# Optimization experiments

Measured on AMD Instinct MI355X. Metric: run time of the kernel, lower is better.

The kernel has to match this reference:

```python
import jax, jax.numpy as jnp
import numpy as np

R, B, N, H = 10, 8, 8192, 8          # ROIs, patients, nodes/ROI-graph, inner hidden
K = N // 2                            # TopKPooling ratio=0.5 -> ceil(0.5*N)
EPAIR = 65536                         # undirected edge pairs per patient graph
E = 2 * B * EPAIR                     # directed edges per ROI (both directions, all patients)
FIN = 4
HEADS, OH = 4, 16
SUPER_DIM = 2 * H + 3                 # (inner_layers+1)*hidden + 3 centroid coords = 19
EPS = 1e-5


def setup_inputs() -> dict:
    key = jax.random.key(0)
    ks = jax.random.split(key, 24)
    roi_x = jax.random.normal(ks[0], (R, B * N, FIN), jnp.float32)
    # within-graph undirected random edges, offset per patient
    u = jax.random.randint(ks[1], (R, B, EPAIR), 0, N)
    v = jax.random.randint(ks[2], (R, B, EPAIR), 0, N)
    off = (jnp.arange(B) * N)[None, :, None]
    src = jnp.concatenate([u + off, v + off], axis=-1).reshape(R, -1)
    dst = jnp.concatenate([v + off, u + off], axis=-1).reshape(R, -1)
    roi_edge_index = jnp.stack([src, dst], axis=1).astype(jnp.int32)  # [R, 2, E]
    centroids = jax.random.uniform(ks[3], (R, B, 3), jnp.float32) + 0.1  # nonzero -> all ROIs kept
    g = lambda k, s: jax.random.normal(k, s, jnp.float32) * 0.1
    return {
        'roi_x': roi_x,
        'roi_edge_index': roi_edge_index,
        'centroids': centroids,
        'gcn_w': g(ks[4], (R, FIN, H)),
        'gcn_b': g(ks[5], (R, H)),
        'ln_w': jnp.ones((R, H), jnp.float32),
        'ln_b': jnp.zeros((R, H), jnp.float32),
        'topk_w': g(ks[6], (R, H)),
        'gat1_w': g(ks[7], (SUPER_DIM, HEADS * OH)),
        'att_src1': g(ks[8], (HEADS, OH)),
        'att_dst1': g(ks[9], (HEADS, OH)),
        'gat1_b': g(ks[10], (HEADS * OH,)),
        'ln_o1_w': jnp.ones((HEADS * OH,), jnp.float32),
        'ln_o1_b': jnp.zeros((HEADS * OH,), jnp.float32),
        'gat2_w': g(ks[11], (HEADS * OH, OH)),
        'att_src2': g(ks[12], (1, OH)),
        'att_dst2': g(ks[13], (1, OH)),
        'gat2_b': g(ks[14], (OH,)),
        'ln_o2_w': jnp.ones((OH,), jnp.float32),
        'ln_o2_b': jnp.zeros((OH,), jnp.float32),
        'lin_w': g(ks[15], (OH, 2)),
        'lin_b': g(ks[16], (2,)),
    }


def _inner_roi(x, edges, cen, Wg, bg, wln, bln, wtk):
    """GCNConv(4,H)+ReLU -> graph-mode LayerNorm -> TopKPooling -> mean pools. x: [B*N, 4]."""
    src, dst = edges[0], edges[1]
    h = x @ Wg                                                     # [BN, H]
    # GCN symmetric norm with self loops: deg = in-degree + 1
    deg = jax.ops.segment_sum(jnp.ones((E,), x.dtype), dst, num_segments=B * N) + 1.0
    dis = deg ** -0.5
    norm = dis[src] * dis[dst]
    agg = jax.ops.segment_sum(h[src] * norm[:, None], dst, num_segments=B * N)
    h = jax.nn.relu(agg + h / deg[:, None] + bg)
    # PyG LayerNorm (mode='graph'): normalize over all nodes & channels per patient graph
    hb = h.reshape(B, N, H)
    mu = hb.mean(axis=(1, 2), keepdims=True)
    var = ((hb - mu) ** 2).mean(axis=(1, 2), keepdims=True)
    hn = (hb - mu) / jnp.sqrt(var + EPS) * wln + bln               # [B, N, H]
    res = hn.mean(axis=1)                                          # residual global_mean_pool [B, H]
    # TopKPooling: score = tanh(x.w/||w||); keep top K per graph; scale kept nodes by score
    s = jnp.tanh(jnp.einsum('bnh,h->bn', hn, wtk) / jnp.linalg.norm(wtk))
    vals, idx = jax.lax.top_k(s, K)                                # [B, K]
    sel = jnp.take_along_axis(hn, idx[:, :, None], axis=1) * vals[:, :, None]
    fv = sel.mean(axis=1)                                          # global_mean_pool after pooling
    return jnp.concatenate([res, fv, cen], axis=1)                 # [B, 19]


def _gat(x, src, dst, W, a_s, a_d, b, heads, oc):
    """PyG GATConv (self loops already included in src/dst)."""
    n = x.shape[0]
    h = (x @ W).reshape(n, heads, oc)
    es = (h * a_s).sum(-1)                                         # [n, heads]
    ed = (h * a_d).sum(-1)
    e = jax.nn.leaky_relu(es[src] + ed[dst], 0.2)                  # [E, heads]
    m = jax.ops.segment_max(e, dst, num_segments=n)
    ex = jnp.exp(e - m[dst])
    den = jax.ops.segment_sum(ex, dst, num_segments=n)
    alpha = ex / den[dst]
    out = jax.ops.segment_sum(h[src] * alpha[:, :, None], dst, num_segments=n)
    return out.reshape(n, heads * oc) + b


def _graph_ln(x, w, b):
    xb = x.reshape(B, R, -1)
    mu = xb.mean(axis=(1, 2), keepdims=True)
    var = ((xb - mu) ** 2).mean(axis=(1, 2), keepdims=True)
    return ((xb - mu) / jnp.sqrt(var + EPS) * w + b).reshape(B * R, -1)


def reference(roi_x, roi_edge_index, centroids, gcn_w, gcn_b, ln_w, ln_b, topk_w,
              gat1_w, att_src1, att_dst1, gat1_b, ln_o1_w, ln_o1_b,
              gat2_w, att_src2, att_dst2, gat2_b, ln_o2_w, ln_o2_b, lin_w, lin_b):
    feats = jax.vmap(_inner_roi)(roi_x, roi_edge_index, centroids,
                                 gcn_w, gcn_b, ln_w, ln_b, topk_w)   # [R, B, 19]
    super_x = feats.transpose(1, 0, 2).reshape(B * R, SUPER_DIM)      # patient-major node order
    # star edges 0->1..9 per patient, plus GATConv's default self loops
    pat = jnp.arange(B) * R
    sl = jnp.arange(B * R)
    ssrc = jnp.concatenate([jnp.repeat(pat, R - 1), sl])
    sdst = jnp.concatenate([(pat[:, None] + jnp.arange(1, R)).reshape(-1), sl])
    x1 = jax.nn.elu(_gat(super_x, ssrc, sdst, gat1_w, att_src1, att_dst1, gat1_b, HEADS, OH))
    x1 = _graph_ln(x1, ln_o1_w, ln_o1_b)
    x2 = jax.nn.elu(_gat(x1, ssrc, sdst, gat2_w, att_src2, att_dst2, gat2_b, 1, OH))
    x2 = _graph_ln(x2, ln_o2_w, ln_o2_b)
    pooled = x2.reshape(B, R, OH).mean(axis=1)                        # global_mean_pool
    # dropout p=0.5 is a no-op in eval mode
    return pooled @ lin_w + lin_b                                     # [B, 2]
```

## Files before the change

kernel.cpp:

```cpp
#include <hip/hip_runtime.h>
#include <hip/hip_bf16.h>
#include <math.h>

#define RR 10
#define BB 8
#define NN 8192
#define HH 8
#define BN 65536
#define EE (1u << 20)
#define EPB (EE / BB)
#define NPAIR (EPB / 2)
#define KK 4096
#define NSUP 80
#define CSRL8 17408

#define NTL(p) __builtin_nontemporal_load(p)
typedef int vi4 __attribute__((ext_vector_type(4)));

__global__ __launch_bounds__(1024)
void count_kernel(const int* __restrict__ ei, const float* __restrict__ x,
                  unsigned char* __restrict__ rankg,
                  unsigned short* __restrict__ qo8g, int* __restrict__ et8g,
                  float* __restrict__ zg) {
  const int bid = blockIdx.x;
  const int rb = bid % 80;
  const int p = bid / 80;
  const int r = rb / BB;
  const int b = rb % BB;
  const int tid = threadIdx.x;

  __shared__ int scnt[1024];
  __shared__ int ps[1024];
  scnt[tid] = 0;
  __syncthreads();

  const int* up = ei + (size_t)r * 2u * EE + (size_t)b * EPB;
  const int* vp = ei + (size_t)r * 2u * EE + EE + (size_t)b * EPB;
  unsigned char* rk = rankg + (size_t)rb * EPB;

#define CNT(U, V, E)                                                \
  {                                                                 \
    int lv = (V) & (NN - 1);                                        \
    if ((lv >> 10) == p) {                                          \
      int t0 = atomicAdd(&scnt[lv & 1023], 1);                      \
      rk[E] = (unsigned char)t0;                                    \
    }                                                               \
    int lu = (U) & (NN - 1);                                        \
    if ((lu >> 10) == p) {                                          \
      int t1 = atomicAdd(&scnt[lu & 1023], 1);                      \
      rk[(E) + NPAIR] = (unsigned char)t1;                          \
    }                                                               \
  }
#pragma unroll 4
  for (int it = 0; it < 16; ++it) {
    int e = it * 4096 + tid * 4;
    vi4 uu = NTL((const vi4*)(up + e));
    vi4 vv = NTL((const vi4*)(vp + e));
    CNT(uu.x, vv.x, e) CNT(uu.y, vv.y, e + 1)
    CNT(uu.z, vv.z, e + 2) CNT(uu.w, vv.w, e + 3)
  }
#undef CNT
  __syncthreads();

  int a = scnt[tid];
  ps[tid] = a;
  __syncthreads();
  for (int s2 = 1; s2 < 1024; s2 <<= 1) {
    int v = 0;
    if (tid >= s2) v = ps[tid - s2];
    __syncthreads();
    ps[tid] += v;
    __syncthreads();
  }
  int incl = ps[tid];
  qo8g[(size_t)rb * 8192 + (size_t)p * 1024 + tid] = (unsigned short)(incl - a);
  if (tid == 1023) et8g[rb * 8 + p] = incl;

  {
    int n = p * 1024 + tid;
    const float4* x4 = (const float4*)x + (size_t)r * BN + (size_t)b * NN;
    float4* z4 = (float4*)zg + (size_t)rb * NN;
    float ds = rsqrtf((float)a + 1.0f);
    float4 xv = x4[n];
    z4[n] = make_float4(xv.x * ds, xv.y * ds, xv.z * ds, xv.w * ds);
  }
}

__global__ __launch_bounds__(512)
void scatfuse_kernel(const int* __restrict__ ei, const float* __restrict__ zg,
                     const unsigned char* __restrict__ rankg,
                     const unsigned short* __restrict__ qo8g, const int* __restrict__ et8g,
                     const float* __restrict__ gcn_w, const float* __restrict__ gcn_b,
                     const float* __restrict__ ln_w, const float* __restrict__ topk_w,
                     float* __restrict__ v4g, float* __restrict__ tg,
                     double* __restrict__ partsS, float* __restrict__ partsC) {
  const int bid = blockIdx.x;
  const int rb = bid % 80;
  const int e8 = bid / 80;
  const int r = rb / BB;
  const int b = rb % BB;
  const int tid = threadIdx.x;

  __shared__ unsigned short qoE[1025];
  __shared__ __align__(16) unsigned short csrL[CSRL8];

  const unsigned short* qo8 = qo8g + (size_t)rb * 8192 + (size_t)e8 * 1024;
  for (int i = tid; i < 1024; i += 512) qoE[i] = qo8[i];
  if (tid == 0) qoE[1024] = (unsigned short)et8g[rb * 8 + e8];
  __syncthreads();

  const int* up = ei + (size_t)r * 2u * EE + (size_t)b * EPB;
  const int* vp = ei + (size_t)r * 2u * EE + EE + (size_t)b * EPB;
  const unsigned char* rk = rankg + (size_t)rb * EPB;

#define SCAT(U, V, RA, RB2)                                         \
  {                                                                 \
    int lv = (V) & (NN - 1);                                        \
    if ((lv >> 10) == e8) {                                         \
      csrL[(int)qoE[lv & 1023] + (int)(RA)] =                       \
          (unsigned short)((U) & (NN - 1));                         \
    }                                                               \
    int lu = (U) & (NN - 1);                                        \
    if ((lu >> 10) == e8) {                                         \
      csrL[(int)qoE[lu & 1023] + (int)(RB2)] =                      \
          (unsigned short)((V) & (NN - 1));                         \
    }                                                               \
  }
#pragma unroll 4
  for (int it = 0; it < 32; ++it) {
    int e = it * 2048 + tid * 4;
    unsigned ra = NTL((const unsigned*)(rk + e));
    unsigned rbv = NTL((const unsigned*)(rk + NPAIR + e));
    vi4 uu = NTL((const vi4*)(up + e));
    vi4 vv = NTL((const vi4*)(vp + e));
    SCAT(uu.x, vv.x, ra & 255u, rbv & 255u)
    SCAT(uu.y, vv.y, (ra >> 8) & 255u, (rbv >> 8) & 255u)
    SCAT(uu.z, vv.z, (ra >> 16) & 255u, (rbv >> 16) & 255u)
    SCAT(uu.w, vv.w, (ra >> 24) & 255u, (rbv >> 24) & 255u)
  }
#undef SCAT
  __syncthreads();

  const float* wp = gcn_w + r * 32;
  const float* bgp = gcn_b + r * 8;
  float lwwt[8];
#pragma unroll
  for (int c = 0; c < 8; ++c) lwwt[c] = ln_w[r * 8 + c] * topk_w[r * 8 + c];

  const float4* z4 = (const float4*)zg + (size_t)rb * NN;
  float4* v4o = (float4*)v4g + (size_t)rb * NN;
  float* trow = tg + (size_t)rb * NN;

  double s1 = 0.0, s2 = 0.0;
  float ch[8] = {0, 0, 0, 0, 0, 0, 0, 0};

#pragma unroll
  for (int k = 0; k < 2; ++k) {
    int idx = tid + k * 512;
    int n = e8 * 1024 + idx;
    int o = (int)qoE[idx];
    int c = (int)qoE[idx + 1] - o;
    float4 zn = z4[n];
    float sx = zn.x, sy = zn.y, sz = zn.z, sw = zn.w;
    int j = 0;
    for (; j + 3 < c; j += 4) {
      int n0 = csrL[o + j], n1 = csrL[o + j + 1], n2 = csrL[o + j + 2], n3 = csrL[o + j + 3];
      float4 a0 = z4[n0], a1 = z4[n1], a2 = z4[n2], a3 = z4[n3];
      sx += a0.x + a1.x + a2.x + a3.x;
      sy += a0.y + a1.y + a2.y + a3.y;
      sz += a0.z + a1.z + a2.z + a3.z;
      sw += a0.w + a1.w + a2.w + a3.w;
    }
    for (; j < c; ++j) {
      int n0 = csrL[o + j];
      float4 a0 = z4[n0];
      sx += a0.x; sy += a0.y; sz += a0.z; sw += a0.w;
    }
    float dd = rsqrtf((float)c + 1.0f);
    float v0 = sx * dd, v1 = sy * dd, v2 = sz * dd, v3 = sw * dd;
    v4o[n] = make_float4(v0, v1, v2, v3);
    float t = 0.f;
#pragma unroll
    for (int cc = 0; cc < 8; ++cc) {
      float h = fmaxf(v0 * wp[cc] + v1 * wp[8 + cc] + v2 * wp[16 + cc] + v3 * wp[24 + cc] + bgp[cc], 0.0f);
      s1 += h;
      s2 += (double)h * h;
      ch[cc] += h;
      t += h * lwwt[cc];
    }
    trow[n] = t;
  }

  __syncthreads();
  double* wredS = (double*)csrL;
  float* wredC = (float*)(csrL + 512);
  int lane = tid & 63, wid = tid >> 6;
#pragma unroll
  for (int off = 32; off > 0; off >>= 1) {
    s1 += __shfl_down(s1, off);
    s2 += __shfl_down(s2, off);
#pragma unroll
    for (int cc = 0; cc < 8; ++cc) ch[cc] += __shfl_down(ch[cc], off);
  }
  if (lane == 0) {
    wredS[wid * 2] = s1;
    wredS[wid * 2 + 1] = s2;
#pragma unroll
    for (int cc = 0; cc < 8; ++cc) wredC[wid * 8 + cc] = ch[cc];
  }
  __syncthreads();
  if (tid == 0) {
    double a = 0.0, b3 = 0.0;
    for (int w2 = 0; w2 < 8; ++w2) { a += wredS[w2 * 2]; b3 += wredS[w2 * 2 + 1]; }
    partsS[bid * 2] = a;
    partsS[bid * 2 + 1] = b3;
  }
  if (tid < 8) {
    float sc = 0.f;
    for (int w2 = 0; w2 < 8; ++w2) sc += wredC[w2 * 8 + tid];
    partsC[bid * 8 + tid] = sc;
  }
}

__global__ __launch_bounds__(1024)
void roiB_kernel(const float* __restrict__ tg, const float* __restrict__ v4g,
                 const double* __restrict__ partsS, const float* __restrict__ partsC,
                 const float* __restrict__ gcn_w, const float* __restrict__ gcn_b,
                 const float* __restrict__ ln_w, const float* __restrict__ ln_b,
                 const float* __restrict__ topk_w, const float* __restrict__ cen,
                 float* __restrict__ feats) {
  const int rb = blockIdx.x;
  const int r = rb / BB;
  const int tid = threadIdx.x;
  const int lane = tid & 63, wid = tid >> 6;

  __shared__ int histW[16 * 256];
  __shared__ int wtot[16];
  __shared__ float chS[8];
  __shared__ float fvSum[8];
  __shared__ int cntGt;
  __shared__ int selb, kleft;
  __shared__ float sstat[2];

  float lw[8], lb[8], wt[8], w[32], bg[8];
  float wn2 = 0.f, L1 = 0.f, B1 = 0.f;
#pragma unroll
  for (int i = 0; i < 32; ++i) w[i] = gcn_w[r * 32 + i];
#pragma unroll
  for (int c = 0; c < 8; ++c) {
    lw[c] = ln_w[r * 8 + c];
    lb[c] = ln_b[r * 8 + c];
    wt[c] = topk_w[r * 8 + c];
    bg[c] = gcn_b[r * 8 + c];
    wn2 += wt[c] * wt[c];
    L1 += lw[c] * wt[c];
    B1 += lb[c] * wt[c];
  }
  const float invn = 1.0f / sqrtf(wn2);

  if (tid == 0) {
    double s1 = 0.0, s2 = 0.0;
    for (int p = 0; p < 8; ++p) {
      s1 += partsS[(p * 80 + rb) * 2];
      s2 += partsS[(p * 80 + rb) * 2 + 1];
    }
    const double M = (double)NN * HH;
    double mu = s1 / M;
    double var = s2 / M - mu * mu;
    sstat[0] = (float)mu;
    sstat[1] = (float)(1.0 / sqrt(var + 1e-5));
    cntGt = 0;
  }
  if (tid < 8) {
    float sc = 0.f;
    for (int p = 0; p < 8; ++p) sc += partsC[(p * 80 + rb) * 8 + tid];
    chS[tid] = sc;
    fvSum[tid] = 0.f;
  }
  __syncthreads();
  const float muf = sstat[0];
  const float rstd = sstat[1];
  const float C0 = B1 - rstd * muf * L1;

  const float* trow = tg + (size_t)rb * NN;
  float sv[8];
  unsigned fl[8];
#pragma unroll
  for (int i = 0; i < 8; ++i) {
    int n = tid * 8 + i;
    float s = tanhf((rstd * trow[n] + C0) * invn);
    sv[i] = s;
    unsigned u = __float_as_uint(s);
    fl[i] = (u & 0x80000000u) ? ~u : (u | 0x80000000u);
  }

  unsigned prefix = 0;
  int kneed = KK;
  for (int shift = 24; shift >= 0; shift -= 8) {
#pragma unroll
    for (int z = 0; z < 4; ++z) histW[tid + z * 1024] = 0;
    __syncthreads();
#pragma unroll
    for (int i = 0; i < 8; ++i) {
      bool m = (shift == 24) || ((fl[i] >> (shift + 8)) == prefix);
      if (m) atomicAdd(&histW[wid * 256 + ((fl[i] >> shift) & 255)], 1);
    }
    __syncthreads();
    if (wid == 0) {
      int b0 = lane * 4;
      int t0 = 0, t1 = 0, t2 = 0, t3 = 0;
      for (int w2 = 0; w2 < 16; ++w2) {
        const int* hp2 = &histW[w2 * 256 + b0];
        t0 += hp2[0]; t1 += hp2[1]; t2 += hp2[2]; t3 += hp2[3];
      }
      int s3 = t3, s2i = t2 + s3, s1i = t1 + s2i, s0 = t0 + s1i;
      int v = s0;
#pragma unroll
      for (int off = 1; off < 64; off <<= 1) {
        int o = __shfl_down(v, off);
        v += (lane + off < 64) ? o : 0;
      }
      int above = v - s0;
      int S3 = above + s3, S2 = above + s2i, S1 = above + s1i, S0 = above + s0;
      if (S3 >= kneed && above < kneed)      { selb = b0 + 3; kleft = kneed - above; }
      else if (S2 >= kneed && S3 < kneed)    { selb = b0 + 2; kleft = kneed - S3; }
      else if (S1 >= kneed && S2 < kneed)    { selb = b0 + 1; kleft = kneed - S2; }
      else if (S0 >= kneed && S1 < kneed)    { selb = b0;     kleft = kneed - S1; }
    }
    __syncthreads();
    prefix = (prefix << 8) | (unsigned)selb;
    kneed = kleft;
  }
  float tau = (prefix & 0x80000000u) ? __uint_as_float(prefix & 0x7fffffffu)
                                     : __uint_as_float(~prefix);

  int cg = 0, ct = 0;
#pragma unroll
  for (int i = 0; i < 8; ++i) {
    if (sv[i] > tau) cg++;
    else if (sv[i] == tau) ct++;
  }
  int wcg = cg;
#pragma unroll
  for (int off = 32; off > 0; off >>= 1) wcg += __shfl_down(wcg, off);
  if (lane == 0) atomicAdd(&cntGt, wcg);
  int sc = ct;
#pragma unroll
  for (int off = 1; off < 64; off <<= 1) {
    int o = __shfl_up(sc, off);
    if (lane >= off) sc += o;
  }
  if (lane == 63) wtot[wid] = sc;
  __syncthreads();
  int wbase = 0;
  for (int w2 = 0; w2 < wid; ++w2) wbase += wtot[w2];
  int rank = wbase + sc - ct;
  int quota = KK - cntGt;

  const float4* v4r = (const float4*)v4g + (size_t)rb * NN;
  float fva[8] = {0, 0, 0, 0, 0, 0, 0, 0};
#pragma unroll
  for (int i = 0; i < 8; ++i) {
    bool inc = sv[i] > tau;
    if (!inc && sv[i] == tau) { inc = (rank < quota); rank++; }
    if (inc) {
      int n = tid * 8 + i;
      float4 vv = v4r[n];
#pragma unroll
      for (int c = 0; c < 8; ++c) {
        float h = fmaxf(vv.x * w[c] + vv.y * w[8 + c] + vv.z * w[16 + c] + vv.w * w[24 + c] + bg[c], 0.0f);
        float hn = (h - muf) * rstd * lw[c] + lb[c];
        fva[c] += hn * sv[i];
      }
    }
  }
#pragma unroll
  for (int c = 0; c < 8; ++c) atomicAdd(&fvSum[c], fva[c]);
  __syncthreads();

  size_t fo = (size_t)rb * 19;
  if (tid < 8) {
    feats[fo + tid] = ((chS[tid] - (float)NN * muf) * rstd * lw[tid]) / (float)NN + lb[tid];
    feats[fo + 8 + tid] = fvSum[tid] / (float)KK;
  }
  if (tid >= 16 && tid < 19) {
    feats[fo + tid] = cen[(size_t)rb * 3 + (tid - 16)];
  }
}

__global__ __launch_bounds__(256)
void super_kernel(const float* __restrict__ feats,
                  const float* __restrict__ W1, const float* __restrict__ as1,
                  const float* __restrict__ ad1, const float* __restrict__ b1,
                  const float* __restrict__ lnw1, const float* __restrict__ lnb1,
                  const float* __restrict__ W2, const float* __restrict__ as2,
                  const float* __restrict__ ad2, const float* __restrict__ b2,
                  const float* __restrict__ lnw2, const float* __restrict__ lnb2,
                  const float* __restrict__ linw, const float* __restrict__ linb,
                  float* __restrict__ out) {
  __shared__ float sx[NSUP * 19];
  __shared__ float h1[NSUP * 64];
  __shared__ float x1[NSUP * 64];
  __shared__ float es1[NSUP * 4], ed1[NSUP * 4];
  __shared__ float h2[NSUP * 16], x2[NSUP * 16];
  __shared__ float es2[NSUP], ed2[NSUP];
  __shared__ float stat[16];
  const int tid = threadIdx.x;

  for (int i = tid; i < NSUP * 19; i += 256) {
    int n = i / 19, c = i % 19;
    int bb = n / RR, rr = n % RR;
    sx[i] = feats[(size_t)(rr * BB + bb) * 19 + c];
  }
  __syncthreads();
  for (int p = tid; p < NSUP * 64; p += 256) {
    int n = p / 64, j = p % 64;
    float acc = 0.f;
    for (int k2 = 0; k2 < 19; ++k2) acc += sx[n * 19 + k2] * W1[k2 * 64 + j];
    h1[p] = acc;
  }
  __syncthreads();
  for (int p = tid; p < NSUP * 4; p += 256) {
    int n = p / 4, hd = p % 4;
    float a = 0.f, d2 = 0.f;
    for (int o = 0; o < 16; ++o) {
      float hv = h1[n * 64 + hd * 16 + o];
      a += hv * as1[hd * 16 + o];
      d2 += hv * ad1[hd * 16 + o];
    }
    es1[p] = a; ed1[p] = d2;
  }
  __syncthreads();
  for (int p = tid; p < NSUP * 64; p += 256) {
    int n = p / 64, j = p % 64, hd = j / 16;
    int rr = n % RR;
    float o;
    if (rr == 0) {
      o = h1[p];
    } else {
      int hub = n - rr;
      float eh = es1[hub * 4 + hd] + ed1[n * 4 + hd];
      float esf = es1[n * 4 + hd] + ed1[n * 4 + hd];
      eh = eh > 0.f ? eh : 0.2f * eh;
      esf = esf > 0.f ? esf : 0.2f * esf;
      float m = fmaxf(eh, esf);
      float wh = expf(eh - m), ws2 = expf(esf - m);
      o = (wh * h1[hub * 64 + j] + ws2 * h1[n * 64 + j]) / (wh + ws2);
    }
    float v = o + b1[j];
    x1[p] = v > 0.f ? v : expm1f(v);
  }
  __syncthreads();
  if (tid < BB) {
    double m = 0.0, v2 = 0.0;
    for (int q = 0; q < RR * 64; ++q) {
      float val = x1[tid * RR * 64 + q];
      m += val; v2 += (double)val * val;
    }
    m /= (RR * 64.0); v2 = v2 / (RR * 64.0) - m * m;
    stat[tid] = (float)m;
    stat[8 + tid] = (float)(1.0 / sqrt(v2 + 1e-5));
  }
  __syncthreads();
  for (int p = tid; p < NSUP * 64; p += 256) {
    int n = p / 64, j = p % 64, bb = n / RR;
    x1[p] = (x1[p] - stat[bb]) * stat[8 + bb] * lnw1[j] + lnb1[j];
  }
  __syncthreads();
  for (int p = tid; p < NSUP * 16; p += 256) {
    int n = p / 16, o = p % 16;
    float acc = 0.f;
    for (int j = 0; j < 64; ++j) acc += x1[n * 64 + j] * W2[j * 16 + o];
    h2[p] = acc;
  }
  __syncthreads();
  for (int n = tid; n < NSUP; n += 256) {
    float a = 0.f, d2 = 0.f;
    for (int o = 0; o < 16; ++o) {
      float hv = h2[n * 16 + o];
      a += hv * as2[o];
      d2 += hv * ad2[o];
    }
    es2[n] = a; ed2[n] = d2;
  }
  __syncthreads();
  for (int p = tid; p < NSUP * 16; p += 256) {
    int n = p / 16, o = p % 16;
    int rr = n % RR;
    float ov;
    if (rr == 0) ov = h2[p];
    else {
      int hub = n - rr;
      float eh = es2[hub] + ed2[n];
      float esf = es2[n] + ed2[n];
      eh = eh > 0.f ? eh : 0.2f * eh;
      esf = esf > 0.f ? esf : 0.2f * esf;
      float m = fmaxf(eh, esf);
      float wh = expf(eh - m), ws2 = expf(esf - m);
      ov = (wh * h2[hub * 16 + o] + ws2 * h2[p]) / (wh + ws2);
    }
    float v = ov + b2[o];
    x2[p] = v > 0.f ? v : expm1f(v);
  }
  __syncthreads();
  if (tid < BB) {
    double m = 0.0, v2 = 0.0;
    for (int q = 0; q < RR * 16; ++q) {
      float val = x2[tid * RR * 16 + q];
      m += val; v2 += (double)val * val;
    }
    m /= (RR * 16.0); v2 = v2 / (RR * 16.0) - m * m;
    stat[tid] = (float)m;
    stat[8 + tid] = (float)(1.0 / sqrt(v2 + 1e-5));
  }
  __syncthreads();
  for (int p = tid; p < NSUP * 16; p += 256) {
    int n = p / 16, o = p % 16, bb = n / RR;
    x2[p] = (x2[p] - stat[bb]) * stat[8 + bb] * lnw2[o] + lnb2[o];
  }
  __syncthreads();
  if (tid < BB * 2) {
    int bb = tid / 2, t = tid % 2;
    float acc = linb[t];
    for (int o = 0; o < 16; ++o) {
      float pm = 0.f;
      for (int rr = 0; rr < RR; ++rr) pm += x2[(bb * RR + rr) * 16 + o];
      pm /= (float)RR;
      acc += pm * linw[o * 2 + t];
    }
    out[bb * 2 + t] = acc;
  }
}

extern "C" void kernel_launch(void* const* d_in, const int* in_sizes, int n_in,
                              void* d_out, int out_size, void* d_ws, size_t ws_size,
                              hipStream_t stream) {
  const float* roi_x = (const float*)d_in[0];
  const int* ei = (const int*)d_in[1];
  const float* cen = (const float*)d_in[2];
  const float* gcn_w = (const float*)d_in[3];
  const float* gcn_b = (const float*)d_in[4];
  const float* ln_w = (const float*)d_in[5];
  const float* ln_b = (const float*)d_in[6];
  const float* topk_w = (const float*)d_in[7];
  const float* gat1_w = (const float*)d_in[8];
  const float* as1 = (const float*)d_in[9];
  const float* ad1 = (const float*)d_in[10];
  const float* b1 = (const float*)d_in[11];
  const float* lnw1 = (const float*)d_in[12];
  const float* lnb1 = (const float*)d_in[13];
  const float* W2 = (const float*)d_in[14];
  const float* as2 = (const float*)d_in[15];
  const float* ad2 = (const float*)d_in[16];
  const float* b2 = (const float*)d_in[17];
  const float* lnw2 = (const float*)d_in[18];
  const float* lnb2 = (const float*)d_in[19];
  const float* linw = (const float*)d_in[20];
  const float* linb = (const float*)d_in[21];
  float* out = (float*)d_out;

  char* wsb = (char*)d_ws;
  float* v4g = (float*)wsb;
  float* zg = (float*)(wsb + (size_t)80 * NN * 4 * 4);
  float* tg = (float*)((char*)zg + (size_t)80 * NN * 4 * 4);
  double* partsS = (double*)((char*)tg + (size_t)80 * NN * 4);
  float* partsC = (float*)((char*)partsS + 1280 * 8);
  unsigned short* qo8 = (unsigned short*)((char*)partsC + 5120 * 4);
  int* et8 = (int*)((char*)qo8 + (size_t)80 * 8192 * 2);
  float* feats = (float*)((char*)et8 + 640 * 4);
  unsigned char* rankg = (unsigned char*)((char*)feats + (size_t)RR * BB * 19 * 4);

  count_kernel<<<640, 1024, 0, stream>>>(ei, roi_x, rankg, qo8, et8, zg);
  scatfuse_kernel<<<640, 512, 0, stream>>>(ei, zg, rankg, qo8, et8,
                                           gcn_w, gcn_b, ln_w, topk_w,
                                           v4g, tg, partsS, partsC);
  roiB_kernel<<<80, 1024, 0, stream>>>(tg, v4g, partsS, partsC,
                                       gcn_w, gcn_b, ln_w, ln_b, topk_w, cen, feats);
  super_kernel<<<1, 256, 0, stream>>>(feats, gat1_w, as1, ad1, b1, lnw1, lnb1,
                                      W2, as2, ad2, b2, lnw2, lnb2, linw, linb, out);
}
```

Baseline: 217.8 us.

## Split degree counting by edge chunk with per-chunk histograms and merge kernel

Degree counting changes from node-range partitioning, where each of 8 blocks per graph scans all edges and keeps only its own node slice, to edge-chunk partitioning, where each block histograms 1/8 of the edges over all 8192 nodes in shared memory. A new merge kernel sums the 8 per-chunk byte histograms, runs the prefix scan and computes the normalized features. The scatter kernel then advances per-node offsets chunk by chunk so the chunk-local ranks stay valid. This removes the 8x redundant read of the edge list in the count phase, at the cost of an extra kernel launch, more shared memory (32 KB histogram), histogram traffic, and extra barriers in the scatter loop. Per-chunk counts are stored as bytes, which assumes no node exceeds 255 incoming edges within one chunk.

```diff
diff --git a/kernel.cpp b/kernel.cpp
--- a/kernel.cpp
+++ b/kernel.cpp
@@ -18,8 +18,46 @@
 typedef int vi4 __attribute__((ext_vector_type(4)));
 
 __global__ __launch_bounds__(1024)
-void count_kernel(const int* __restrict__ ei, const float* __restrict__ x,
-                  unsigned char* __restrict__ rankg,
+void count_kernel(const int* __restrict__ ei, unsigned char* __restrict__ rankg,
+                  unsigned char* __restrict__ Hg) {
+  const int bid = blockIdx.x;
+  const int rb = bid % 80;
+  const int c = bid / 80;
+  const int r = rb / BB;
+  const int b = rb % BB;
+  const int tid = threadIdx.x;
+
+  __shared__ int hist[NN];
+  for (int i = tid; i < NN; i += 1024) hist[i] = 0;
+  __syncthreads();
+
+  const int* up = ei + (size_t)r * 2u * EE + (size_t)b * EPB;
+  const int* vp = ei + (size_t)r * 2u * EE + EE + (size_t)b * EPB;
+  unsigned char* rk = rankg + (size_t)rb * EPB;
+
+#pragma unroll
+  for (int it = 0; it < 2; ++it) {
+    int e = c * 8192 + it * 4096 + tid * 4;
+    vi4 uu = NTL((const vi4*)(up + e));
+    vi4 vv = NTL((const vi4*)(vp + e));
+#define DO(j, U, V)                                                 \
+    {                                                               \
+      int r0 = atomicAdd(&hist[(V) & (NN - 1)], 1);                 \
+      rk[e + (j)] = (unsigned char)r0;                              \
+      int r1 = atomicAdd(&hist[(U) & (NN - 1)], 1);                 \
+      rk[e + (j) + NPAIR] = (unsigned char)r1;                      \
+    }
+    DO(0, uu.x, vv.x) DO(1, uu.y, vv.y) DO(2, uu.z, vv.z) DO(3, uu.w, vv.w)
+#undef DO
+  }
+  __syncthreads();
+
+  unsigned char* hg = Hg + ((size_t)rb * 8 + c) * NN;
+  for (int i = tid; i < NN; i += 1024) hg[i] = (unsigned char)hist[i];
+}
+
+__global__ __launch_bounds__(1024)
+void merge_kernel(const unsigned char* __restrict__ Hg, const float* __restrict__ x,
                   unsigned short* __restrict__ qo8g, int* __restrict__ et8g,
                   float* __restrict__ zg) {
   const int bid = blockIdx.x;
@@ -29,41 +67,14 @@
   const int b = rb % BB;
   const int tid = threadIdx.x;
 
-  __shared__ int scnt[1024];
   __shared__ int ps[1024];
-  scnt[tid] = 0;
-  __syncthreads();
-
-  const int* up = ei + (size_t)r * 2u * EE + (size_t)b * EPB;
-  const int* vp = ei + (size_t)r * 2u * EE + EE + (size_t)b * EPB;
-  unsigned char* rk = rankg + (size_t)rb * EPB;
-
-#define CNT(U, V, E)                                                \
-  {                                                                 \
-    int lv = (V) & (NN - 1);                                        \
-    if ((lv >> 10) == p) {                                          \
-      int t0 = atomicAdd(&scnt[lv & 1023], 1);                      \
-      rk[E] = (unsigned char)t0;                                    \
-    }                                                               \
-    int lu = (U) & (NN - 1);                                        \
-    if ((lu >> 10) == p) {                                          \
-      int t1 = atomicAdd(&scnt[lu & 1023], 1);                      \
-      rk[(E) + NPAIR] = (unsigned char)t1;                          \
-    }                                                               \
-  }
-#pragma unroll 4
-  for (int it = 0; it < 16; ++it) {
-    int e = it * 4096 + tid * 4;
-    vi4 uu = NTL((const vi4*)(up + e));
-    vi4 vv = NTL((const vi4*)(vp + e));
-    CNT(uu.x, vv.x, e) CNT(uu.y, vv.y, e + 1)
-    CNT(uu.z, vv.z, e + 2) CNT(uu.w, vv.w, e + 3)
-  }
-#undef CNT
-  __syncthreads();
-
-  int a = scnt[tid];
-  ps[tid] = a;
+  int n = p * 1024 + tid;
+  const unsigned char* hg = Hg + (size_t)rb * 8 * NN;
+  int deg = 0;
+#pragma unroll
+  for (int c = 0; c < 8; ++c) deg += (int)hg[(size_t)c * NN + n];
+
+  ps[tid] = deg;
   __syncthreads();
   for (int s2 = 1; s2 < 1024; s2 <<= 1) {
     int v = 0;
@@ -73,23 +84,21 @@
     __syncthreads();
   }
   int incl = ps[tid];
-  qo8g[(size_t)rb * 8192 + (size_t)p * 1024 + tid] = (unsigned short)(incl - a);
+  qo8g[(size_t)rb * 8192 + (size_t)p * 1024 + tid] = (unsigned short)(incl - deg);
   if (tid == 1023) et8g[rb * 8 + p] = incl;
 
-  {
-    int n = p * 1024 + tid;
-    const float4* x4 = (const float4*)x + (size_t)r * BN + (size_t)b * NN;
-    float4* z4 = (float4*)zg + (size_t)rb * NN;
-    float ds = rsqrtf((float)a + 1.0f);
-    float4 xv = x4[n];
-    z4[n] = make_float4(xv.x * ds, xv.y * ds, xv.z * ds, xv.w * ds);
-  }
+  const float4* x4 = (const float4*)x + (size_t)r * BN + (size_t)b * NN;
+  float4* z4 = (float4*)zg + (size_t)rb * NN;
+  float ds = rsqrtf((float)deg + 1.0f);
+  float4 xv = x4[n];
+  z4[n] = make_float4(xv.x * ds, xv.y * ds, xv.z * ds, xv.w * ds);
 }
 
 __global__ __launch_bounds__(512)
 void scatfuse_kernel(const int* __restrict__ ei, const float* __restrict__ zg,
                      const unsigned char* __restrict__ rankg,
                      const unsigned short* __restrict__ qo8g, const int* __restrict__ et8g,
+                     const unsigned char* __restrict__ Hg,
                      const float* __restrict__ gcn_w, const float* __restrict__ gcn_b,
                      const float* __restrict__ ln_w, const float* __restrict__ topk_w,
                      float* __restrict__ v4g, float* __restrict__ tg,
@@ -102,44 +111,55 @@
   const int tid = threadIdx.x;
 
   __shared__ unsigned short qoE[1025];
+  __shared__ unsigned short qoCur[1024];
   __shared__ __align__(16) unsigned short csrL[CSRL8];
 
   const unsigned short* qo8 = qo8g + (size_t)rb * 8192 + (size_t)e8 * 1024;
-  for (int i = tid; i < 1024; i += 512) qoE[i] = qo8[i];
+  for (int i = tid; i < 1024; i += 512) {
+    unsigned short v = qo8[i];
+    qoE[i] = v;
+    qoCur[i] = v;
+  }
   if (tid == 0) qoE[1024] = (unsigned short)et8g[rb * 8 + e8];
   __syncthreads();
 
   const int* up = ei + (size_t)r * 2u * EE + (size_t)b * EPB;
   const int* vp = ei + (size_t)r * 2u * EE + EE + (size_t)b * EPB;
   const unsigned char* rk = rankg + (size_t)rb * EPB;
+  const unsigned char* hg = Hg + (size_t)rb * 8 * NN + (size_t)e8 * 1024;
 
 #define SCAT(U, V, RA, RB2)                                         \
   {                                                                 \
     int lv = (V) & (NN - 1);                                        \
     if ((lv >> 10) == e8) {                                         \
-      csrL[(int)qoE[lv & 1023] + (int)(RA)] =                       \
+      csrL[(int)qoCur[lv & 1023] + (int)(RA)] =                     \
           (unsigned short)((U) & (NN - 1));                         \
     }                                                               \
     int lu = (U) & (NN - 1);                                        \
     if ((lu >> 10) == e8) {                                         \
-      csrL[(int)qoE[lu & 1023] + (int)(RB2)] =                      \
+      csrL[(int)qoCur[lu & 1023] + (int)(RB2)] =                    \
           (unsigned short)((V) & (NN - 1));                         \
     }                                                               \
   }
-#pragma unroll 4
-  for (int it = 0; it < 32; ++it) {
-    int e = it * 2048 + tid * 4;
-    unsigned ra = NTL((const unsigned*)(rk + e));
-    unsigned rbv = NTL((const unsigned*)(rk + NPAIR + e));
-    vi4 uu = NTL((const vi4*)(up + e));
-    vi4 vv = NTL((const vi4*)(vp + e));
-    SCAT(uu.x, vv.x, ra & 255u, rbv & 255u)
-    SCAT(uu.y, vv.y, (ra >> 8) & 255u, (rbv >> 8) & 255u)
-    SCAT(uu.z, vv.z, (ra >> 16) & 255u, (rbv >> 16) & 255u)
-    SCAT(uu.w, vv.w, (ra >> 24) & 255u, (rbv >> 24) & 255u)
+  for (int c = 0; c < 8; ++c) {
+#pragma unroll
+    for (int it = 0; it < 4; ++it) {
+      int e = c * 8192 + it * 2048 + tid * 4;
+      unsigned ra = NTL((const unsigned*)(rk + e));
+      unsigned rbv = NTL((const unsigned*)(rk + NPAIR + e));
+      vi4 uu = NTL((const vi4*)(up + e));
+      vi4 vv = NTL((const vi4*)(vp + e));
+      SCAT(uu.x, vv.x, ra & 255u, rbv & 255u)
+      SCAT(uu.y, vv.y, (ra >> 8) & 255u, (rbv >> 8) & 255u)
+      SCAT(uu.z, vv.z, (ra >> 16) & 255u, (rbv >> 16) & 255u)
+      SCAT(uu.w, vv.w, (ra >> 24) & 255u, (rbv >> 24) & 255u)
+    }
+    __syncthreads();
+    for (int i = tid; i < 1024; i += 512)
+      qoCur[i] = (unsigned short)((int)qoCur[i] + (int)hg[(size_t)c * NN + i]);
+    __syncthreads();
   }
 #undef SCAT
-  __syncthreads();
 
   const float* wp = gcn_w + r * 32;
   const float* bgp = gcn_b + r * 8;
@@ -569,9 +589,11 @@
   int* et8 = (int*)((char*)qo8 + (size_t)80 * 8192 * 2);
   float* feats = (float*)((char*)et8 + 640 * 4);
   unsigned char* rankg = (unsigned char*)((char*)feats + (size_t)RR * BB * 19 * 4);
-
-  count_kernel<<<640, 1024, 0, stream>>>(ei, roi_x, rankg, qo8, et8, zg);
-  scatfuse_kernel<<<640, 512, 0, stream>>>(ei, zg, rankg, qo8, et8,
+  unsigned char* Hg = rankg + (size_t)80 * EPB;
+
+  count_kernel<<<640, 1024, 0, stream>>>(ei, rankg, Hg);
+  merge_kernel<<<640, 1024, 0, stream>>>(Hg, roi_x, qo8, et8, zg);
+  scatfuse_kernel<<<640, 512, 0, stream>>>(ei, zg, rankg, qo8, et8, Hg,
                                            gcn_w, gcn_b, ln_w, topk_w,
                                            v4g, tg, partsS, partsC);
   roiB_kernel<<<80, 1024, 0, stream>>>(tg, v4g, partsS, partsC,
```

New measurement: 181.0 us (median of 2 runs). 1.2x faster.
